# Optimization experiments

Measured on AMD Instinct MI355X. Metric: run time of the kernel, lower is better.

The kernel has to match this reference:

```python
import jax, jax.numpy as jnp
import numpy as np

DOMAIN_MIN, DOMAIN_MAX = -1.0, 1.0
N, D_IN, D_OUT, K = 1024, 128, 128, 8


def setup_inputs() -> dict:
    key = jax.random.key(0)
    k1, k2, k3 = jax.random.split(key, 3)
    x = jax.random.uniform(k1, (N, D_IN), dtype=jnp.float32,
                           minval=DOMAIN_MIN, maxval=DOMAIN_MAX)
    # Per-edge spline knot values: near-identity init plus small noise.
    base = jnp.linspace(DOMAIN_MIN, DOMAIN_MAX, K, dtype=jnp.float32)
    coeffs = base[None, None, :] + 0.1 * jax.random.normal(
        k2, (D_OUT, D_IN, K), dtype=jnp.float32)
    weights = jax.random.normal(k3, (D_OUT, D_IN), dtype=jnp.float32) * np.sqrt(2.0 / D_IN)
    bias = jnp.zeros((D_OUT,), dtype=jnp.float32)
    return {"x": x, "coeffs": coeffs, "weights": weights, "bias": bias}


def _spline_all_edges(x, coeffs):
    """Evaluate every edge's cubic (Catmull-Rom) spline at its input.
    x: [N, d_in]; coeffs: [d_out, d_in, K] knot values on uniform knots in [-1,1].
    Returns s: [N, d_in, d_out]."""
    K_ = coeffs.shape[-1]
    h = (DOMAIN_MAX - DOMAIN_MIN) / (K_ - 1)
    xc = jnp.clip(x, DOMAIN_MIN, DOMAIN_MAX)
    t = (xc - DOMAIN_MIN) / h                      # [N, d_in], in [0, K-1]
    idx = jnp.clip(jnp.floor(t).astype(jnp.int32), 0, K_ - 2)
    u = t - idx                                    # local coord in [0,1]
    i0 = jnp.clip(idx - 1, 0, K_ - 1)
    i1 = idx
    i2 = idx + 1
    i3 = jnp.clip(idx + 2, 0, K_ - 1)
    ct = jnp.transpose(coeffs, (1, 2, 0))          # [d_in, K, d_out]
    jar = jnp.arange(ct.shape[0])[None, :]          # [1, d_in]
    p0 = ct[jar, i0]                               # [N, d_in, d_out]
    p1 = ct[jar, i1]
    p2 = ct[jar, i2]
    p3 = ct[jar, i3]
    u2 = u * u
    u3 = u2 * u
    b0 = 0.5 * (-u3 + 2.0 * u2 - u)
    b1 = 0.5 * (3.0 * u3 - 5.0 * u2 + 2.0)
    b2 = 0.5 * (-3.0 * u3 + 4.0 * u2 + u)
    b3 = 0.5 * (u3 - u2)
    return (b0[..., None] * p0 + b1[..., None] * p1 +
            b2[..., None] * p2 + b3[..., None] * p3)


def reference(x, coeffs, weights, bias):
    # h_i(x) = sum_j w_ij * s_ij(x_j) + b_i
    s = _spline_all_edges(x, coeffs)               # [N, d_in, d_out]
    return jnp.einsum('njo,oj->no', s, weights) + bias[None, :]
```

## Files before the change

### kernel.cpp

```cpp
#include <hip/hip_runtime.h>
#include <hip/hip_bf16.h>
#include <stdint.h>


#define DIN 128
#define DOUT 128
#define KTOT 1024

typedef unsigned int u32;
typedef unsigned short u16;
typedef __attribute__((ext_vector_type(8))) short bf16x8;
typedef __attribute__((ext_vector_type(4))) float f32x4;

union H8 { u16 s[8]; uint4 v; };

__device__ __forceinline__ u16 f2b(float f) {
    union { __hip_bfloat16 h; u16 u; } c;
    c.h = __float2bfloat16(f);
    return c.u;
}

__global__ __launch_bounds__(256) void kan_prep(
    const float* __restrict__ x, const float* __restrict__ coeffs,
    const float* __restrict__ weights, u16* __restrict__ ws0,
    u16* __restrict__ ws1)
{
    const int tid = threadIdx.x;
    if (blockIdx.x < 512) {
        const int task = blockIdx.x * 256 + tid;
        float xv = x[task];
        xv = fminf(fmaxf(xv, -1.0f), 1.0f);
        const float t = (xv + 1.0f) * 3.5f;
        int idx = (int)t; idx = idx > 6 ? 6 : idx;
        const float u = t - (float)idx;
        const float u2 = u * u, u3 = u2 * u;
        const float b0 = 0.5f * (-u3 + 2.0f * u2 - u);
        const float b1 = 0.5f * (3.0f * u3 - 5.0f * u2 + 2.0f);
        const float b2 = 0.5f * (-3.0f * u3 + 4.0f * u2 + u);
        const float b3 = 0.5f * (u3 - u2);
        float r[8];
        #pragma unroll
        for (int k = 0; k < 8; ++k) r[k] = 0.0f;
        const int i0 = idx > 0 ? idx - 1 : 0;
        const int i3 = idx < 6 ? idx + 2 : 7;
        r[i0] += b0; r[idx] += b1; r[idx + 1] += b2; r[i3] += b3;
        H8 h;
        #pragma unroll
        for (int k = 0; k < 8; ++k) h.s[k] = f2b(r[k]);
        *(uint4*)(ws0 + task * 8) = h.v;
    } else {
        const int task = (blockIdx.x - 512) * 256 + tid;
        const float wv = weights[task];
        const float4 c0 = *(const float4*)(coeffs + task * 8);
        const float4 c1 = *(const float4*)(coeffs + task * 8 + 4);
        H8 h;
        h.s[0] = f2b(c0.x * wv); h.s[1] = f2b(c0.y * wv);
        h.s[2] = f2b(c0.z * wv); h.s[3] = f2b(c0.w * wv);
        h.s[4] = f2b(c1.x * wv); h.s[5] = f2b(c1.y * wv);
        h.s[6] = f2b(c1.z * wv); h.s[7] = f2b(c1.w * wv);
        *(uint4*)(ws1 + task * 8) = h.v;
    }
}

__global__ __launch_bounds__(256) void kan_gemm(
    const u16* __restrict__ ws0, const u16* __restrict__ ws1,
    const float* __restrict__ bias, float* __restrict__ out)
{
    __shared__ float sC[4 * 256];

    const int tid  = threadIdx.x;
    const int wave = tid >> 6;
    const int lane = tid & 63;
    const int mo = lane & 15;
    const int q  = lane >> 4;
    const int n0 = blockIdx.x * 16;
    const int o0 = blockIdx.y * 16;

    const u16* ap = ws0 + (n0 + mo) * KTOT + wave * 256 + q * 8;
    const u16* bp = ws1 + (o0 + mo) * KTOT + wave * 256 + q * 8;

    f32x4 acc = {0.0f, 0.0f, 0.0f, 0.0f};
    #pragma unroll
    for (int s = 0; s < 8; ++s) {
        bf16x8 af = *(const bf16x8*)(ap + s * 32);
        bf16x8 bf = *(const bf16x8*)(bp + s * 32);
        acc = __builtin_amdgcn_mfma_f32_16x16x32_bf16(af, bf, acc, 0, 0, 0);
    }

    #pragma unroll
    for (int r = 0; r < 4; ++r)
        sC[wave * 256 + (q * 4 + r) * 16 + mo] = acc[r];
    __syncthreads();

    const int row = tid >> 4, col = tid & 15;
    float v = sC[tid] + sC[256 + tid] + sC[512 + tid] + sC[768 + tid];
    out[(n0 + row) * DOUT + o0 + col] = v + bias[o0 + col];
}

extern "C" void kernel_launch(void* const* d_in, const int* in_sizes, int n_in,
                              void* d_out, int out_size, void* d_ws, size_t ws_size,
                              hipStream_t stream) {
    const float* x       = (const float*)d_in[0];
    const float* coeffs  = (const float*)d_in[1];
    const float* weights = (const float*)d_in[2];
    const float* bias    = (const float*)d_in[3];
    float* out = (float*)d_out;
    u16* ws0 = (u16*)d_ws;
    u16* ws1 = ws0 + 1024 * KTOT;
    kan_prep<<<576, 256, 0, stream>>>(x, coeffs, weights, ws0, ws1);
    dim3 grid(1024 / 16, DOUT / 16);
    kan_gemm<<<grid, 256, 0, stream>>>(ws0, ws1, bias, out);
}
```

Baseline: 65.28 us.

## Fuse basis/weight prep into GEMM kernel using swizzled shared memory tiles

Merges the prep and GEMM kernels into one. Each block builds its 16-row basis tile and 16-output weighted-coefficient tile directly in XOR-swizzled LDS, then runs the MFMA loop from shared memory. This removes the second launch and the global workspace round trip for the intermediate bf16 matrices. In exchange, each block recomputes the basis rows (8x redundancy across o-blocks) and the weight tiles (64x across n-blocks), and uses 64KB of LDS per block, which limits occupancy.

```diff
diff --git a/kernel.cpp b/kernel.cpp
--- a/kernel.cpp
+++ b/kernel.cpp
@@ -20,15 +20,27 @@
     return c.u;
 }
 
-__global__ __launch_bounds__(256) void kan_prep(
+__global__ __launch_bounds__(256) void kan_fused(
     const float* __restrict__ x, const float* __restrict__ coeffs,
-    const float* __restrict__ weights, u16* __restrict__ ws0,
-    u16* __restrict__ ws1)
+    const float* __restrict__ weights, const float* __restrict__ bias,
+    float* __restrict__ out)
 {
-    const int tid = threadIdx.x;
-    if (blockIdx.x < 512) {
-        const int task = blockIdx.x * 256 + tid;
-        float xv = x[task];
+    __shared__ __align__(16) u16 sBas[16 * KTOT];
+    __shared__ __align__(16) u16 sWp [16 * KTOT];
+    float* sC = (float*)sBas;
+
+    const int tid  = threadIdx.x;
+    const int wave = tid >> 6;
+    const int lane = tid & 63;
+    const int n0 = blockIdx.x * 16;
+    const int o0 = blockIdx.y * 16;
+
+    #pragma unroll
+    for (int it = 0; it < 8; ++it) {
+        const int task = tid + it * 256;
+        const int row = task >> 7;
+        const int j = task & 127;
+        float xv = x[n0 * DIN + task];
         xv = fminf(fmaxf(xv, -1.0f), 1.0f);
         const float t = (xv + 1.0f) * 3.5f;
         int idx = (int)t; idx = idx > 6 ? 6 : idx;
@@ -47,45 +59,41 @@
         H8 h;
         #pragma unroll
         for (int k = 0; k < 8; ++k) h.s[k] = f2b(r[k]);
-        *(uint4*)(ws0 + task * 8) = h.v;
-    } else {
-        const int task = (blockIdx.x - 512) * 256 + tid;
-        const float wv = weights[task];
-        const float4 c0 = *(const float4*)(coeffs + task * 8);
-        const float4 c1 = *(const float4*)(coeffs + task * 8 + 4);
+        const int uu = j ^ (row & 7);
+        *(uint4*)(sBas + row * KTOT + uu * 8) = h.v;
+    }
+
+    #pragma unroll
+    for (int it = 0; it < 8; ++it) {
+        const int task = tid + it * 256;
+        const int o = task >> 7;
+        const int j = task & 127;
+        const float wv = weights[o0 * DIN + task];
+        const float4 c0 = *(const float4*)(coeffs + o0 * KTOT + task * 8);
+        const float4 c1 = *(const float4*)(coeffs + o0 * KTOT + task * 8 + 4);
         H8 h;
         h.s[0] = f2b(c0.x * wv); h.s[1] = f2b(c0.y * wv);
         h.s[2] = f2b(c0.z * wv); h.s[3] = f2b(c0.w * wv);
         h.s[4] = f2b(c1.x * wv); h.s[5] = f2b(c1.y * wv);
         h.s[6] = f2b(c1.z * wv); h.s[7] = f2b(c1.w * wv);
-        *(uint4*)(ws1 + task * 8) = h.v;
+        const int uu = j ^ (o & 7);
+        *(uint4*)(sWp + o * KTOT + uu * 8) = h.v;
     }
-}
+    __syncthreads();
 
-__global__ __launch_bounds__(256) void kan_gemm(
-    const u16* __restrict__ ws0, const u16* __restrict__ ws1,
-    const float* __restrict__ bias, float* __restrict__ out)
-{
-    __shared__ float sC[4 * 256];
-
-    const int tid  = threadIdx.x;
-    const int wave = tid >> 6;
-    const int lane = tid & 63;
     const int mo = lane & 15;
     const int q  = lane >> 4;
-    const int n0 = blockIdx.x * 16;
-    const int o0 = blockIdx.y * 16;
-
-    const u16* ap = ws0 + (n0 + mo) * KTOT + wave * 256 + q * 8;
-    const u16* bp = ws1 + (o0 + mo) * KTOT + wave * 256 + q * 8;
-
+    const int sw = mo & 7;
     f32x4 acc = {0.0f, 0.0f, 0.0f, 0.0f};
     #pragma unroll
     for (int s = 0; s < 8; ++s) {
-        bf16x8 af = *(const bf16x8*)(ap + s * 32);
-        bf16x8 bf = *(const bf16x8*)(bp + s * 32);
+        const int S = wave * 8 + s;
+        const int uu = (S * 4 + q) ^ sw;
+        bf16x8 af = *(const bf16x8*)(sBas + mo * KTOT + uu * 8);
+        bf16x8 bf = *(const bf16x8*)(sWp  + mo * KTOT + uu * 8);
         acc = __builtin_amdgcn_mfma_f32_16x16x32_bf16(af, bf, acc, 0, 0, 0);
     }
+    __syncthreads();
 
     #pragma unroll
     for (int r = 0; r < 4; ++r)
@@ -105,9 +113,7 @@
     const float* weights = (const float*)d_in[2];
     const float* bias    = (const float*)d_in[3];
     float* out = (float*)d_out;
-    u16* ws0 = (u16*)d_ws;
-    u16* ws1 = ws0 + 1024 * KTOT;
-    kan_prep<<<576, 256, 0, stream>>>(x, coeffs, weights, ws0, ws1);
-    dim3 grid(1024 / 16, DOUT / 16);
-    kan_gemm<<<grid, 256, 0, stream>>>(ws0, ws1, bias, out);
+    const int N = in_sizes[0] / DIN;
+    dim3 grid(N / 16, DOUT / 16);
+    kan_fused<<<grid, 256, 0, stream>>>(x, coeffs, weights, bias, out);
 }
```

Result: faster. 63.33 us (-3.0%).

## Fuse prep and GEMM into one split-K kernel with atomic accumulation

Applied to the files above, without the earlier changes.

Removes the global workspace round trip by computing the spline basis and the weighted coefficients per tile directly in shared memory, using an XOR swizzle, then doing one MFMA per wave. The input dimension is split across blockIdx.z (8 slices), and partial results go to the output with float atomics after a memset. In exchange the basis and coefficient prep is recomputed redundantly across output tiles, launch count grows (memset plus 4096 blocks), and atomics add contention and non-deterministic summation order.

```diff
diff --git a/kernel.cpp b/kernel.cpp
--- a/kernel.cpp
+++ b/kernel.cpp
@@ -20,15 +20,26 @@
     return c.u;
 }
 
-__global__ __launch_bounds__(256) void kan_prep(
+__global__ __launch_bounds__(256, 8) void kan_slice(
     const float* __restrict__ x, const float* __restrict__ coeffs,
-    const float* __restrict__ weights, u16* __restrict__ ws0,
-    u16* __restrict__ ws1)
+    const float* __restrict__ weights, const float* __restrict__ bias,
+    float* __restrict__ out)
 {
-    const int tid = threadIdx.x;
-    if (blockIdx.x < 512) {
-        const int task = blockIdx.x * 256 + tid;
-        float xv = x[task];
+    __shared__ __align__(16) u16 sBas[16 * 128];
+    __shared__ __align__(16) u16 sWp [16 * 128];
+    __shared__ float sC[4 * 256];
+
+    const int tid  = threadIdx.x;
+    const int wave = tid >> 6;
+    const int lane = tid & 63;
+    const int n0 = blockIdx.x * 16;
+    const int o0 = blockIdx.y * 16;
+    const int js = blockIdx.z * 16;
+
+    {
+        const int row = tid >> 4;
+        const int jl = tid & 15;
+        float xv = x[(n0 + row) * DIN + js + jl];
         xv = fminf(fmaxf(xv, -1.0f), 1.0f);
         const float t = (xv + 1.0f) * 3.5f;
         int idx = (int)t; idx = idx > 6 ? 6 : idx;
@@ -47,54 +58,46 @@
         H8 h;
         #pragma unroll
         for (int k = 0; k < 8; ++k) h.s[k] = f2b(r[k]);
-        *(uint4*)(ws0 + task * 8) = h.v;
-    } else {
-        const int task = (blockIdx.x - 512) * 256 + tid;
-        const float wv = weights[task];
-        const float4 c0 = *(const float4*)(coeffs + task * 8);
-        const float4 c1 = *(const float4*)(coeffs + task * 8 + 4);
+        const int uu = jl ^ (row & 7);
+        *(uint4*)(sBas + row * 128 + uu * 8) = h.v;
+    }
+
+    {
+        const int o = tid >> 4;
+        const int jl = tid & 15;
+        const float wv = weights[(o0 + o) * DIN + js + jl];
+        const float* cp = coeffs + (o0 + o) * KTOT + (js + jl) * 8;
+        const float4 c0 = *(const float4*)(cp);
+        const float4 c1 = *(const float4*)(cp + 4);
         H8 h;
         h.s[0] = f2b(c0.x * wv); h.s[1] = f2b(c0.y * wv);
         h.s[2] = f2b(c0.z * wv); h.s[3] = f2b(c0.w * wv);
         h.s[4] = f2b(c1.x * wv); h.s[5] = f2b(c1.y * wv);
         h.s[6] = f2b(c1.z * wv); h.s[7] = f2b(c1.w * wv);
-        *(uint4*)(ws1 + task * 8) = h.v;
+        const int uu = jl ^ (o & 7);
+        *(uint4*)(sWp + o * 128 + uu * 8) = h.v;
     }
-}
+    __syncthreads();
 
-__global__ __launch_bounds__(256) void kan_gemm(
-    const u16* __restrict__ ws0, const u16* __restrict__ ws1,
-    const float* __restrict__ bias, float* __restrict__ out)
-{
-    __shared__ float sC[4 * 256];
-
-    const int tid  = threadIdx.x;
-    const int wave = tid >> 6;
-    const int lane = tid & 63;
     const int mo = lane & 15;
     const int q  = lane >> 4;
-    const int n0 = blockIdx.x * 16;
-    const int o0 = blockIdx.y * 16;
-
-    const u16* ap = ws0 + (n0 + mo) * KTOT + wave * 256 + q * 8;
-    const u16* bp = ws1 + (o0 + mo) * KTOT + wave * 256 + q * 8;
-
+    const int uu = (wave * 4 + q) ^ (mo & 7);
+    bf16x8 af = *(const bf16x8*)(sBas + mo * 128 + uu * 8);
+    bf16x8 bf = *(const bf16x8*)(sWp  + mo * 128 + uu * 8);
     f32x4 acc = {0.0f, 0.0f, 0.0f, 0.0f};
-    #pragma unroll
-    for (int s = 0; s < 8; ++s) {
-        bf16x8 af = *(const bf16x8*)(ap + s * 32);
-        bf16x8 bf = *(const bf16x8*)(bp + s * 32);
-        acc = __builtin_amdgcn_mfma_f32_16x16x32_bf16(af, bf, acc, 0, 0, 0);
-    }
+    acc = __builtin_amdgcn_mfma_f32_16x16x32_bf16(af, bf, acc, 0, 0, 0);
 
     #pragma unroll
     for (int r = 0; r < 4; ++r)
         sC[wave * 256 + (q * 4 + r) * 16 + mo] = acc[r];
     __syncthreads();
 
-    const int row = tid >> 4, col = tid & 15;
-    float v = sC[tid] + sC[256 + tid] + sC[512 + tid] + sC[768 + tid];
-    out[(n0 + row) * DOUT + o0 + col] = v + bias[o0 + col];
+    {
+        const int row = tid >> 4, col = tid & 15;
+        float v = sC[tid] + sC[256 + tid] + sC[512 + tid] + sC[768 + tid];
+        if (blockIdx.z == 0) v += bias[o0 + col];
+        atomicAdd(out + (n0 + row) * DOUT + o0 + col, v);
+    }
 }
 
 extern "C" void kernel_launch(void* const* d_in, const int* in_sizes, int n_in,
@@ -105,9 +108,7 @@
     const float* weights = (const float*)d_in[2];
     const float* bias    = (const float*)d_in[3];
     float* out = (float*)d_out;
-    u16* ws0 = (u16*)d_ws;
-    u16* ws1 = ws0 + 1024 * KTOT;
-    kan_prep<<<576, 256, 0, stream>>>(x, coeffs, weights, ws0, ws1);
-    dim3 grid(1024 / 16, DOUT / 16);
-    kan_gemm<<<grid, 256, 0, stream>>>(ws0, ws1, bias, out);
+    hipMemsetAsync(out, 0, (size_t)out_size * sizeof(float), stream);
+    dim3 grid(1024 / 16, DOUT / 16, DIN / 16);
+    kan_slice<<<grid, 256, 0, stream>>>(x, coeffs, weights, bias, out);
 }
```

Measured after the change: 65.81 us. About the same (+0.8%).
